# Optimization experiments

Hardware: AMD Instinct MI355X
Metric: run time of the kernel (lower is better)

## Reference

```python
import jax, jax.numpy as jnp
import numpy as np

IN_F = 2048
OUT_F = 2048
N_ROWS = 8192


def _perm(n):
    # t_o(n) is a permutation matrix P with P[i, p(i)] = 1, p(i) = (4i mod n) + (4i // n)
    i = np.arange(n)
    return (4 * i) % n + (4 * i) // n


def _inv(p):
    inv = np.empty_like(p)
    inv[p] = np.arange(len(p))
    return inv

# (P_in^T @ H)[a, :] = H[i, :] where p_in(i) = a  ->  rows indexed by inv(p_in)
_INV_P_IN = _inv(_perm(IN_F))
# (H @ P_out)[:, b] = H[:, j] where p_out(j) = b  ->  cols indexed by inv(p_out)
_INV_P_OUT = _inv(_perm(OUT_F))


def make_quaternion_mul(kernel):
    # kernel: (in//4, out); split along dim 1 into quaternion components
    r, i, j, k = jnp.split(kernel, 4, axis=1)
    r2 = jnp.concatenate([r, -i, -j, -k], axis=1)
    i2 = jnp.concatenate([i, r, -k, j], axis=1)
    j2 = jnp.concatenate([j, k, r, -i], axis=1)
    k2 = jnp.concatenate([k, -j, i, r], axis=1)
    return jnp.concatenate([r2, i2, j2, k2], axis=0)  # (in, out)


def setup_inputs() -> dict:
    key = jax.random.key(0)
    k1, k2, k3 = jax.random.split(key, 3)
    inp = jax.random.normal(k1, (N_ROWS, IN_F), dtype=jnp.float32)
    weight = jax.random.normal(k2, (IN_F // 4, OUT_F), dtype=jnp.float32) * (1.0 / np.sqrt(IN_F // 4))
    bias = jax.random.normal(k3, (OUT_F,), dtype=jnp.float32) * 0.01
    return {"input": inp, "weight": weight, "bias": bias}


def reference(input, weight, bias):
    hamilton = make_quaternion_mul(weight)                 # (in, out)
    # swap=True: hamilton = L^T @ hamilton @ R, both pure permutations
    hamilton = hamilton[_INV_P_IN][:, _INV_P_OUT]
    support = input @ hamilton + bias[None, :]             # (N, out)
    return support
```

## Files before the change

kernel.cpp:

```cpp
#include <hip/hip_runtime.h>
#include <stdint.h>

#define IN_F 2048
#define OUT_F 2048
#define N_ROWS 8192

#define BM 256
#define BN 256
#define BK 32
#define NT (IN_F / BK)
#define TM_TILES (N_ROWS / BM)
#define TN_TILES (OUT_F / BN)
#define NWG (TM_TILES * TN_TILES)
#define TILE_SHORTS (BM * BK)
#define BUF_SHORTS (2 * TILE_SHORTS)

typedef __bf16 bf16x8 __attribute__((ext_vector_type(8)));
typedef float f32x4 __attribute__((ext_vector_type(4)));
typedef unsigned short ushortx8 __attribute__((ext_vector_type(8)));

__device__ __forceinline__ unsigned short f2bf(float f) {
  unsigned u = __builtin_bit_cast(unsigned, f);
  u += 0x7FFFu + ((u >> 16) & 1u);
  return (unsigned short)(u >> 16);
}

__device__ __forceinline__ void async16(void* lds, const void* g) {
  __builtin_amdgcn_global_load_lds(
      (const __attribute__((address_space(1))) void*)(uintptr_t)g,
      (__attribute__((address_space(3))) void*)(uint32_t)(uintptr_t)lds,
      16, 0, 0);
}

__device__ __forceinline__ bf16x8 ld8(const unsigned short* p) {
  return __builtin_bit_cast(bf16x8, *reinterpret_cast<const ushortx8*>(p));
}

__global__ __launch_bounds__(256) void k_prep(const float* __restrict__ A,
                                              unsigned short* __restrict__ AbT,
                                              const float* __restrict__ W,
                                              unsigned short* __restrict__ BtT) {
  const int bid = blockIdx.x;
  if (bid < 8192) {
    const int tile = bid >> 2;
    const int t = ((bid & 3) << 8) + threadIdx.x;
    const int r = t >> 2;
    const int ga = (t & 3) ^ ((r >> 1) & 3);
    const int R = tile >> 6, T = tile & 63;
    const float* src = A + (size_t)(R * 256 + r) * IN_F + T * 32 + ga * 8;
    const float4 v0 = *reinterpret_cast<const float4*>(src);
    const float4 v1 = *reinterpret_cast<const float4*>(src + 4);
    ushortx8 o;
    o[0] = f2bf(v0.x); o[1] = f2bf(v0.y); o[2] = f2bf(v0.z); o[3] = f2bf(v0.w);
    o[4] = f2bf(v1.x); o[5] = f2bf(v1.y); o[6] = f2bf(v1.z); o[7] = f2bf(v1.w);
    *reinterpret_cast<ushortx8*>(AbT + (size_t)tile * 8192 + t * 8) = o;
  } else {
    const int bb = bid - 8192;
    const int tile = bb >> 2;
    const int t = ((bb & 3) << 8) + threadIdx.x;
    const int r = t >> 2;
    const int ga = (t & 3) ^ ((r >> 1) & 3);
    const int Ct = tile >> 6, T = tile & 63;
    const int b = Ct * 256 + r;
    const int c = b & 3, v = b >> 2;
    const int a0 = T * 32 + ga * 8;
    ushortx8 o;
#pragma unroll
    for (int e = 0; e < 8; ++e) {
      const int a = a0 + e;
      const int q = a & 3, u = a >> 2;
      float w = W[(size_t)u * OUT_F + ((q ^ c) << 9) + v];
      if ((0x284E >> ((q << 2) | c)) & 1) w = -w;
      o[e] = f2bf(w);
    }
    *reinterpret_cast<ushortx8*>(BtT + (size_t)tile * 8192 + t * 8) = o;
  }
}

__global__ __launch_bounds__(512, 2) void k_gemm(const unsigned short* __restrict__ AbT,
                                                 const unsigned short* __restrict__ BtT,
                                                 const float* __restrict__ bias,
                                                 float* __restrict__ C) {
  __shared__ __align__(16) unsigned short lds[5 * BUF_SHORTS];

  const int tid = threadIdx.x;
  const int lane = tid & 63;
  const int w = tid >> 6;
  const int wm = w >> 2;
  const int wn = w & 3;
  const int fr = lane & 15;
  const int g = lane >> 4;

  const int wg = blockIdx.x;
  const int swz = (wg & 7) * (NWG >> 3) + (wg >> 3);
  const int tm = swz >> 3;
  const int tn = swz & 7;
  const int row0 = tm * BM, col0 = tn * BN;

  const unsigned short* baseA = AbT + (size_t)tm * 64 * 8192;
  const unsigned short* baseB = BtT + (size_t)tn * 64 * 8192;
  const int tOff0 = (w * 128 + lane) * 8;
  const int tOff1 = (w * 128 + 64 + lane) * 8;

#define STAGE(T, BUF)                                              \
  do {                                                             \
    unsigned short* base_ = &lds[(BUF) * BUF_SHORTS];              \
    const unsigned short* sa_ = baseA + (size_t)(T) * 8192;        \
    const unsigned short* sb_ = baseB + (size_t)(T) * 8192;        \
    async16(base_ + tOff0, sa_ + tOff0);                           \
    async16(base_ + tOff1, sa_ + tOff1);                           \
    async16(base_ + TILE_SHORTS + tOff0, sb_ + tOff0);             \
    async16(base_ + TILE_SHORTS + tOff1, sb_ + tOff1);             \
  } while (0)

  int offA[8], offB[4];
#pragma unroll
  for (int m = 0; m < 8; ++m) {
    const int r = wm * 128 + m * 16 + fr;
    offA[m] = r * BK + ((g ^ ((r >> 1) & 3)) << 3);
  }
#pragma unroll
  for (int n = 0; n < 4; ++n) {
    const int r = wn * 64 + n * 16 + fr;
    offB[n] = TILE_SHORTS + r * BK + ((g ^ ((r >> 1) & 3)) << 3);
  }

  f32x4 acc[8][4] = {};

#define MFMA_(a_, b_, c_) __builtin_amdgcn_mfma_f32_16x16x32_bf16(a_, b_, c_, 0, 0, 0)

#define WINDOW(T, B0, B1, S0, S1, VMSTR, NS)                                  \
  do {                                                                        \
    asm volatile("s_waitcnt vmcnt(" VMSTR ")" ::: "memory");                  \
    __builtin_amdgcn_s_barrier();                                             \
    __builtin_amdgcn_sched_barrier(0);                                        \
    const unsigned short* p0_ = &lds[(B0) * BUF_SHORTS];                      \
    const unsigned short* p1_ = &lds[(B1) * BUF_SHORTS];                      \
    bf16x8 bg0[4], bg1[4], af0[8], af1[8];                                    \
    _Pragma("unroll") for (int n = 0; n < 4; ++n) bg0[n] = ld8(p0_ + offB[n]);\
    _Pragma("unroll") for (int m = 0; m < 8; ++m) af0[m] = ld8(p0_ + offA[m]);\
    if ((NS) >= 1) STAGE((T) + 3, S0);                                        \
    if ((NS) >= 2) STAGE((T) + 4, S1);                                        \
    _Pragma("unroll") for (int n = 0; n < 4; ++n) bg1[n] = ld8(p1_ + offB[n]);\
    _Pragma("unroll") for (int m = 0; m < 8; ++m) af1[m] = ld8(p1_ + offA[m]);\
    __builtin_amdgcn_s_setprio(1);                                            \
    _Pragma("unroll") for (int m = 0; m < 8; ++m)                             \
      _Pragma("unroll") for (int n = 0; n < 4; ++n)                           \
        acc[m][n] = MFMA_(af0[m], bg0[n], acc[m][n]);                         \
    _Pragma("unroll") for (int m = 0; m < 8; ++m)                             \
      _Pragma("unroll") for (int n = 0; n < 4; ++n)                           \
        acc[m][n] = MFMA_(af1[m], bg1[n], acc[m][n]);                         \
    __builtin_amdgcn_s_setprio(0);                                            \
  } while (0)

  STAGE(0, 0);
  STAGE(1, 1);
  STAGE(2, 2);

#pragma unroll 1
  for (int tb = 0; tb < NT - 4; tb += 10) {
    WINDOW(tb + 0, 0, 1, 3, 4, "4", 2);
    WINDOW(tb + 2, 2, 3, 0, 1, "4", 2);
    WINDOW(tb + 4, 4, 0, 2, 3, "4", 2);
    WINDOW(tb + 6, 1, 2, 4, 0, "4", 2);
    WINDOW(tb + 8, 3, 4, 1, 2, "4", 2);
  }
  WINDOW(NT - 4, 0, 1, 3, 3, "4", 1);
  WINDOW(NT - 2, 2, 3, 0, 0, "0", 0);

#undef WINDOW
#undef STAGE

  const int g4 = g << 2;
  float bv[4];
#pragma unroll
  for (int n = 0; n < 4; ++n) bv[n] = bias[col0 + wn * 64 + n * 16 + fr];
#pragma unroll
  for (int m = 0; m < 8; ++m) {
#pragma unroll
    for (int e = 0; e < 4; ++e) {
      const int row = row0 + wm * 128 + m * 16 + g4 + e;
      float* cp = C + (size_t)row * OUT_F + col0 + wn * 64 + fr;
#pragma unroll
      for (int n = 0; n < 4; ++n) cp[n * 16] = acc[m][n][e] + bv[n];
    }
  }
}

__global__ __launch_bounds__(256) void k_naive(const float* __restrict__ A,
                                               const float* __restrict__ W,
                                               const float* __restrict__ bias,
                                               float* __restrict__ C) {
  const int idx = blockIdx.x * 256 + threadIdx.x;
  const int m = idx >> 11;
  const int b = idx & (OUT_F - 1);
  const int c = b & 3, v = b >> 2;
  float acc = 0.f;
  const float* arow = A + (size_t)m * IN_F;
  for (int a = 0; a < IN_F; ++a) {
    const int q = a & 3, u = a >> 2;
    float h = W[(size_t)u * OUT_F + ((q ^ c) << 9) + v];
    if ((0x284E >> ((q << 2) | c)) & 1) h = -h;
    acc += arow[a] * h;
  }
  C[idx] = acc + bias[b];
}

extern "C" void kernel_launch(void* const* d_in, const int* in_sizes, int n_in,
                              void* d_out, int out_size, void* d_ws, size_t ws_size,
                              hipStream_t stream) {
  (void)in_sizes; (void)n_in; (void)out_size;
  const float* inp  = (const float*)d_in[0];
  const float* w    = (const float*)d_in[1];
  const float* bias = (const float*)d_in[2];
  float* out = (float*)d_out;

  const size_t needA = (size_t)N_ROWS * IN_F * sizeof(unsigned short);
  const size_t needB = (size_t)IN_F * OUT_F * sizeof(unsigned short);
  if (ws_size < needA + needB) {
    k_naive<<<(N_ROWS * OUT_F) / 256, 256, 0, stream>>>(inp, w, bias, out);
    return;
  }

  unsigned short* AbT = (unsigned short*)d_ws;
  unsigned short* BtT = AbT + (size_t)N_ROWS * IN_F;

  k_prep<<<8192 + 2048, 256, 0, stream>>>(inp, AbT, w, BtT);
  k_gemm<<<NWG, 512, 0, stream>>>(AbT, BtT, bias, out);
}
```

Baseline: 93.60 us.

## Software-pipeline LDS fragment reads with double-buffered registers across K steps

Replaces the two-tile window, which loaded both tiles' fragments from LDS before issuing MFMAs, with a per-tile step that computes on fragments already held in registers while the next tile's fragments load into an alternate register set. sched_group_barrier hints interleave the LDS reads and global staging with the MFMAs. The aim is to hide LDS latency behind matrix math and halve the work between barriers. The cost is a second fragment register set and twice as many barriers, with a risk to occupancy and to correctness of the vmcnt waits in the prologue and tail.

```diff
diff --git a/kernel.cpp b/kernel.cpp
--- a/kernel.cpp
+++ b/kernel.cpp
@@ -126,49 +126,71 @@
   }
 
   f32x4 acc[8][4] = {};
+  bf16x8 afE[8], bgE[4], afO[8], bgO[4];
 
 #define MFMA_(a_, b_, c_) __builtin_amdgcn_mfma_f32_16x16x32_bf16(a_, b_, c_, 0, 0, 0)
 
-#define WINDOW(T, B0, B1, S0, S1, VMSTR, NS)                                  \
-  do {                                                                        \
-    asm volatile("s_waitcnt vmcnt(" VMSTR ")" ::: "memory");                  \
-    __builtin_amdgcn_s_barrier();                                             \
-    __builtin_amdgcn_sched_barrier(0);                                        \
-    const unsigned short* p0_ = &lds[(B0) * BUF_SHORTS];                      \
-    const unsigned short* p1_ = &lds[(B1) * BUF_SHORTS];                      \
-    bf16x8 bg0[4], bg1[4], af0[8], af1[8];                                    \
-    _Pragma("unroll") for (int n = 0; n < 4; ++n) bg0[n] = ld8(p0_ + offB[n]);\
-    _Pragma("unroll") for (int m = 0; m < 8; ++m) af0[m] = ld8(p0_ + offA[m]);\
-    if ((NS) >= 1) STAGE((T) + 3, S0);                                        \
-    if ((NS) >= 2) STAGE((T) + 4, S1);                                        \
-    _Pragma("unroll") for (int n = 0; n < 4; ++n) bg1[n] = ld8(p1_ + offB[n]);\
-    _Pragma("unroll") for (int m = 0; m < 8; ++m) af1[m] = ld8(p1_ + offA[m]);\
-    __builtin_amdgcn_s_setprio(1);                                            \
-    _Pragma("unroll") for (int m = 0; m < 8; ++m)                             \
-      _Pragma("unroll") for (int n = 0; n < 4; ++n)                           \
-        acc[m][n] = MFMA_(af0[m], bg0[n], acc[m][n]);                         \
-    _Pragma("unroll") for (int m = 0; m < 8; ++m)                             \
-      _Pragma("unroll") for (int n = 0; n < 4; ++n)                           \
-        acc[m][n] = MFMA_(af1[m], bg1[n], acc[m][n]);                         \
-    __builtin_amdgcn_s_setprio(0);                                            \
+#define STEP(T, SN, SS, AFC, BGC, AFN, BGN, VMSTR, DOSTAGE, DOREAD)            \
+  do {                                                                         \
+    asm volatile("s_waitcnt vmcnt(" VMSTR ")" ::: "memory");                   \
+    __builtin_amdgcn_s_barrier();                                              \
+    __builtin_amdgcn_sched_barrier(0);                                         \
+    if (DOSTAGE) STAGE((T) + 3, SS);                                           \
+    if (DOREAD) {                                                              \
+      const unsigned short* pn_ = &lds[(SN) * BUF_SHORTS];                     \
+      _Pragma("unroll") for (int n = 0; n < 4; ++n)                            \
+          BGN[n] = ld8(pn_ + offB[n]);                                         \
+      _Pragma("unroll") for (int m = 0; m < 8; ++m)                            \
+          AFN[m] = ld8(pn_ + offA[m]);                                         \
+    }                                                                          \
+    __builtin_amdgcn_s_setprio(1);                                             \
+    _Pragma("unroll") for (int m = 0; m < 8; ++m)                              \
+      _Pragma("unroll") for (int n = 0; n < 4; ++n)                            \
+        acc[m][n] = MFMA_(AFC[m], BGC[n], acc[m][n]);                          \
+    __builtin_amdgcn_s_setprio(0);                                             \
+    if (DOSTAGE) __builtin_amdgcn_sched_group_barrier(0x010, 4, 0);            \
+    if (DOREAD) {                                                              \
+      _Pragma("unroll") for (int i_ = 0; i_ < 12; ++i_) {                      \
+        __builtin_amdgcn_sched_group_barrier(0x008, 2, 0);                     \
+        __builtin_amdgcn_sched_group_barrier(0x100, 1, 0);                     \
+      }                                                                        \
+      __builtin_amdgcn_sched_group_barrier(0x008, 8, 0);                       \
+    }                                                                          \
+    __builtin_amdgcn_sched_barrier(0);                                         \
   } while (0)
 
   STAGE(0, 0);
   STAGE(1, 1);
   STAGE(2, 2);
+  asm volatile("s_waitcnt vmcnt(8)" ::: "memory");
+  __builtin_amdgcn_s_barrier();
+  {
+    const unsigned short* p0_ = &lds[0];
+#pragma unroll
+    for (int n = 0; n < 4; ++n) bgE[n] = ld8(p0_ + offB[n]);
+#pragma unroll
+    for (int m = 0; m < 8; ++m) afE[m] = ld8(p0_ + offA[m]);
+  }
 
 #pragma unroll 1
-  for (int tb = 0; tb < NT - 4; tb += 10) {
-    WINDOW(tb + 0, 0, 1, 3, 4, "4", 2);
-    WINDOW(tb + 2, 2, 3, 0, 1, "4", 2);
-    WINDOW(tb + 4, 4, 0, 2, 3, "4", 2);
-    WINDOW(tb + 6, 1, 2, 4, 0, "4", 2);
-    WINDOW(tb + 8, 3, 4, 1, 2, "4", 2);
-  }
-  WINDOW(NT - 4, 0, 1, 3, 3, "4", 1);
-  WINDOW(NT - 2, 2, 3, 0, 0, "0", 0);
-
-#undef WINDOW
+  for (int t0 = 0; t0 < NT - 4; t0 += 10) {
+    STEP(t0 + 0, 1, 3, afE, bgE, afO, bgO, "4", 1, 1);
+    STEP(t0 + 1, 2, 4, afO, bgO, afE, bgE, "4", 1, 1);
+    STEP(t0 + 2, 3, 0, afE, bgE, afO, bgO, "4", 1, 1);
+    STEP(t0 + 3, 4, 1, afO, bgO, afE, bgE, "4", 1, 1);
+    STEP(t0 + 4, 0, 2, afE, bgE, afO, bgO, "4", 1, 1);
+    STEP(t0 + 5, 1, 3, afO, bgO, afE, bgE, "4", 1, 1);
+    STEP(t0 + 6, 2, 4, afE, bgE, afO, bgO, "4", 1, 1);
+    STEP(t0 + 7, 3, 0, afO, bgO, afE, bgE, "4", 1, 1);
+    STEP(t0 + 8, 4, 1, afE, bgE, afO, bgO, "4", 1, 1);
+    STEP(t0 + 9, 0, 2, afO, bgO, afE, bgE, "4", 1, 1);
+  }
+  STEP(NT - 4, 1, 3, afE, bgE, afO, bgO, "4", 1, 1);
+  STEP(NT - 3, 2, 0, afO, bgO, afE, bgE, "4", 0, 1);
+  STEP(NT - 2, 3, 0, afE, bgE, afO, bgO, "0", 0, 1);
+  STEP(NT - 1, 4, 0, afO, bgO, afE, bgE, "0", 0, 0);
+
+#undef STEP
 #undef STAGE
 
   const int g4 = g << 2;
```

New measurement: 90.60 us. -3.2%, faster.
